# Kernel optimization log

Hardware: AMD Instinct MI355X
Metric: run time of the kernel (lower is better)

The kernel has to match this reference:

```python
import jax, jax.numpy as jnp
import numpy as np

E, N, NB = 250000, 20000, 8
D_EDGE, D_RBF, D_CBF, D_TRI = 128, 16, 16, 64
INV_SQRT_2 = 1.0 / np.sqrt(2.0).astype(np.float32)
INV_SQRT_NB = 1.0 / np.sqrt(float(NB))


def setup_inputs() -> dict:
    key = jax.random.key(0)
    ks = jax.random.split(key, 13)
    def w(k, fi, fo):
        return (jax.random.normal(k, (fi, fo), dtype=jnp.float32) / np.sqrt(fi)).astype(jnp.float32)
    return {
        "m_st": jax.random.normal(ks[0], (E, D_EDGE), dtype=jnp.float32),
        "rbf": jax.random.normal(ks[1], (E, D_RBF), dtype=jnp.float32),
        "cbf": jax.random.normal(ks[2], (E, NB, D_CBF), dtype=jnp.float32),
        "idx_s": jax.random.randint(ks[3], (E,), 0, N),
        "idx_swap": jax.random.randint(ks[4], (E,), 0, E),
        "basis_idx1": jax.random.randint(ks[5], (N, NB), 0, E),
        "W_m_rbf": w(ks[6], D_EDGE, D_EDGE),
        "W_rbf": w(ks[7], D_RBF, D_EDGE),
        "W_m_cbf": w(ks[8], D_EDGE, D_TRI),
        "W_cbf": w(ks[9], D_CBF, D_TRI),
        "W_dir": w(ks[10], D_TRI, D_EDGE),
        "W_st": w(ks[11], D_EDGE, D_EDGE),
        "W_ts": w(ks[12], D_EDGE, D_EDGE),
    }


def reference(m_st, rbf, cbf, idx_s, idx_swap, basis_idx1,
              W_m_rbf, W_rbf, W_m_cbf, W_cbf, W_dir, W_st, W_ts):
    act = jax.nn.silu
    # gather per-edge basis indices: (E, NB) -> (E*NB,)
    b1 = basis_idx1[idx_s].reshape(-1)
    # rbf branch (ScaleFactor == 1.0 at init -> identity)
    m = act(m_st @ W_m_rbf)                     # (E, D_EDGE)
    m = m * (rbf @ W_rbf)                       # (E, D_EDGE)
    # cbf branch
    e, nb, c = cbf.shape
    cbf2 = cbf.reshape(e * nb, c)               # (E*NB, D_CBF)
    m_nb = act(m @ W_m_cbf)                     # (E, D_TRI)
    m_nb = m_nb[b1]                             # gather -> (E*NB, D_TRI)
    m_nb = m_nb * (cbf2 @ W_cbf)                # (E*NB, D_TRI)
    x = m_nb.reshape(e, nb, -1).sum(1) * INV_SQRT_NB  # (E, D_TRI)
    x = act(x @ W_dir)                          # (E, D_EDGE)
    x_st = act(x @ W_st)
    x_ts = act(x @ W_ts)[idx_swap]              # swap-gather
    return (x_st + x_ts) * INV_SQRT_2
```

## Files before the change

kernel.cpp:

```cpp
#include <hip/hip_runtime.h>


#define DEV __device__ __forceinline__

typedef __attribute__((ext_vector_type(8))) short bf16x8;
typedef __attribute__((ext_vector_type(4))) float f32x4;

constexpr int E = 250000;
constexpr float INV_SQRT_2  = 0.70710678118654752f;
constexpr float INV_SQRT_NB = 0.35355339059327373f;

constexpr int PW1 = 0;
constexpr int PW2 = 16384;
constexpr int PW3 = 20480;
constexpr int PWD = 28672;
constexpr int PWS = 36864;
constexpr int PWT = 53248;
constexpr int PWC = 69632;
constexpr int PACK_TOTAL = 72192;

constexpr size_t OFF_T = 1u << 18;
constexpr size_t OFF_Z = OFF_T + (size_t)E * 64 * 2;
constexpr size_t WS_NEED_FAST = OFF_Z + (size_t)E * 128 * 4;

DEV unsigned short f2bf(float f) {
  unsigned u = __float_as_uint(f);
  return (unsigned short)((u + 0x7fffu + ((u >> 16) & 1u)) >> 16);
}
DEV float bf2f(unsigned short h) { return __uint_as_float((unsigned)h << 16); }
DEV float silu_f(float x) { return x / (1.f + __expf(-x)); }

__global__ __launch_bounds__(256) void k0_pack(
    const float* __restrict__ W1, const float* __restrict__ W2,
    const float* __restrict__ W3, const float* __restrict__ Wc,
    const float* __restrict__ Wd, const float* __restrict__ Ws,
    const float* __restrict__ Wt, unsigned short* __restrict__ pack) {
  int idx = blockIdx.x * 256 + threadIdx.x;
  if (idx >= PACK_TOTAL) return;
  float v = 0.f;
  if (idx < PW2)      { int i = idx;       int n = i >> 7, k = i & 127; v = W1[k * 128 + n]; }
  else if (idx < PW3) { int i = idx - PW2; int n = i >> 5, k = i & 31;  v = (k < 16) ? W2[k * 128 + n] : 0.f; }
  else if (idx < PWD) { int i = idx - PW3; int n = i >> 7, k = i & 127; v = W3[k * 64 + n]; }
  else if (idx < PWS) { int i = idx - PWD; int n = i >> 6, k = i & 63;  v = Wd[k * 128 + n]; }
  else if (idx < PWT) { int i = idx - PWS; int n = i >> 7, k = i & 127; v = Ws[k * 128 + n]; }
  else if (idx < PWC) { int i = idx - PWT; int n = i >> 7, k = i & 127; v = Wt[k * 128 + n]; }
  else                { int i = idx - PWC; int n = i / 40, k = i % 40;  v = (k < 16) ? Wc[k * 64 + n] : 0.f; }
  pack[idx] = f2bf(v);
}

__global__ __launch_bounds__(512) void k1_mbranch(
    const float* __restrict__ m_st, const float* __restrict__ rbf,
    const unsigned short* __restrict__ pack, unsigned short* __restrict__ tT) {
  __shared__ __align__(16) unsigned short sA[128 * 136];
  __shared__ __align__(16) unsigned short sR[128 * 40];
  const int tid = threadIdx.x;
  const int e0 = blockIdx.x * 128;

  #pragma unroll
  for (int it = 0; it < 16; ++it) {
    int i = tid + it * 512;
    int row = i >> 6, kh = i & 63;
    int er = min(e0 + row, E - 1);
    const float2 v = *(const float2*)(m_st + (size_t)er * 128 + kh * 2);
    unsigned pk = (unsigned)f2bf(v.x) | ((unsigned)f2bf(v.y) << 16);
    *(unsigned*)(sA + row * 136 + kh * 2) = pk;
  }
  #pragma unroll
  for (int it = 0; it < 4; ++it) {
    int i = tid + it * 512;
    int row = i >> 4, kh = i & 15;
    int er = min(e0 + row, E - 1);
    unsigned pk = 0;
    if (kh < 8) {
      const float2 v = *(const float2*)(rbf + (size_t)er * 16 + kh * 2);
      pk = (unsigned)f2bf(v.x) | ((unsigned)f2bf(v.y) << 16);
    }
    *(unsigned*)(sR + row * 40 + kh * 2) = pk;
  }
  __syncthreads();

  const int lane = tid & 63, wv = tid >> 6;
  const int m = lane & 15, q = lane >> 4;
  const int arow = wv * 16 + m;

  const f32x4 zero4 = {0.f, 0.f, 0.f, 0.f};
  f32x4 macc[8], racc[8];
  #pragma unroll
  for (int nt = 0; nt < 8; ++nt) { macc[nt] = zero4; racc[nt] = zero4; }

  {
    bf16x8 a = *(const bf16x8*)(sR + arow * 40 + q * 8);
    #pragma unroll
    for (int nt = 0; nt < 8; ++nt) {
      bf16x8 b = *(const bf16x8*)(pack + PW2 + (nt * 16 + m) * 32 + q * 8);
      racc[nt] = __builtin_amdgcn_mfma_f32_16x16x32_bf16(a, b, racc[nt], 0, 0, 0);
    }
  }
  #pragma unroll
  for (int kk = 0; kk < 4; ++kk) {
    bf16x8 a = *(const bf16x8*)(sA + arow * 136 + kk * 32 + q * 8);
    #pragma unroll
    for (int nt = 0; nt < 8; ++nt) {
      bf16x8 b = *(const bf16x8*)(pack + PW1 + (nt * 16 + m) * 128 + kk * 32 + q * 8);
      macc[nt] = __builtin_amdgcn_mfma_f32_16x16x32_bf16(a, b, macc[nt], 0, 0, 0);
    }
  }
  #pragma unroll
  for (int nt = 0; nt < 8; ++nt)
    #pragma unroll
    for (int r = 0; r < 4; ++r) {
      float v = silu_f(macc[nt][r]) * racc[nt][r];
      sA[(wv * 16 + q * 4 + r) * 136 + nt * 16 + m] = f2bf(v);
    }
  __syncthreads();

  f32x4 tacc[4];
  #pragma unroll
  for (int nt = 0; nt < 4; ++nt) tacc[nt] = zero4;
  #pragma unroll
  for (int kk = 0; kk < 4; ++kk) {
    bf16x8 a = *(const bf16x8*)(sA + arow * 136 + kk * 32 + q * 8);
    #pragma unroll
    for (int nt = 0; nt < 4; ++nt) {
      bf16x8 b = *(const bf16x8*)(pack + PW3 + (nt * 16 + m) * 128 + kk * 32 + q * 8);
      tacc[nt] = __builtin_amdgcn_mfma_f32_16x16x32_bf16(a, b, tacc[nt], 0, 0, 0);
    }
  }
  #pragma unroll
  for (int r = 0; r < 4; ++r) {
    int erow = e0 + wv * 16 + q * 4 + r;
    if (erow < E) {
      ushort4 o;
      o.x = f2bf(silu_f(tacc[0][r]));
      o.y = f2bf(silu_f(tacc[1][r]));
      o.z = f2bf(silu_f(tacc[2][r]));
      o.w = f2bf(silu_f(tacc[3][r]));
      *(ushort4*)(tT + (size_t)erow * 64 + m * 4) = o;
    }
  }
}

DEV void xtile_gather_reduce(
    const float* __restrict__ cbf, const int* __restrict__ sB,
    const unsigned short* __restrict__ tT, const bf16x8* bw,
    unsigned short* __restrict__ sX,
    int wv, int m, int q, long long rowA, long long rowB, int mt) {
  bf16x8 af = {0, 0, 0, 0, 0, 0, 0, 0};
  if (q < 2) {
    long long row = (m < 8) ? rowA + m : rowB + (m - 8);
    const float4 c0 = *(const float4*)(cbf + row * 16 + q * 8);
    const float4 c1 = *(const float4*)(cbf + row * 16 + q * 8 + 4);
    af[0] = (short)f2bf(c0.x); af[1] = (short)f2bf(c0.y);
    af[2] = (short)f2bf(c0.z); af[3] = (short)f2bf(c0.w);
    af[4] = (short)f2bf(c1.x); af[5] = (short)f2bf(c1.y);
    af[6] = (short)f2bf(c1.z); af[7] = (short)f2bf(c1.w);
  }
  const f32x4 zero4 = {0.f, 0.f, 0.f, 0.f};
  f32x4 p0 = zero4, p1 = zero4, p2 = zero4, p3 = zero4;
  p0 = __builtin_amdgcn_mfma_f32_16x16x32_bf16(af, bw[0], p0, 0, 0, 0);
  p1 = __builtin_amdgcn_mfma_f32_16x16x32_bf16(af, bw[1], p1, 0, 0, 0);
  p2 = __builtin_amdgcn_mfma_f32_16x16x32_bf16(af, bw[2], p2, 0, 0, 0);
  p3 = __builtin_amdgcn_mfma_f32_16x16x32_bf16(af, bw[3], p3, 0, 0, 0);

  float s0 = 0.f, s1 = 0.f, s2 = 0.f, s3 = 0.f;
  const int lrb = wv * 128 + mt * 16;
  #pragma unroll
  for (int r = 0; r < 4; ++r) {
    int brow = sB[lrb + q * 4 + r];
    ushort4 tv = *(const ushort4*)(tT + (size_t)brow * 64 + m * 4);
    s0 += bf2f(tv.x) * p0[r];
    s1 += bf2f(tv.y) * p1[r];
    s2 += bf2f(tv.z) * p2[r];
    s3 += bf2f(tv.w) * p3[r];
  }
  s0 += __shfl_xor(s0, 16);
  s1 += __shfl_xor(s1, 16);
  s2 += __shfl_xor(s2, 16);
  s3 += __shfl_xor(s3, 16);

  int lrow = wv * 16 + mt * 2 + (q >> 1);
  if (q == 0 || q == 2) {
    sX[lrow * 72 +  0 + m] = f2bf(s0 * INV_SQRT_NB);
    sX[lrow * 72 + 16 + m] = f2bf(s1 * INV_SQRT_NB);
    sX[lrow * 72 + 32 + m] = f2bf(s2 * INV_SQRT_NB);
    sX[lrow * 72 + 48 + m] = f2bf(s3 * INV_SQRT_NB);
  }
}

DEV void ytile(const unsigned short* __restrict__ pack,
               const unsigned short* __restrict__ sX,
               unsigned short* __restrict__ sY, int wv, int m, int q) {
  const int arow = wv * 16 + m;
  const f32x4 zero4 = {0.f, 0.f, 0.f, 0.f};
  f32x4 yacc[8];
  #pragma unroll
  for (int nt = 0; nt < 8; ++nt) yacc[nt] = zero4;
  #pragma unroll
  for (int kk = 0; kk < 2; ++kk) {
    bf16x8 a = *(const bf16x8*)(sX + arow * 72 + kk * 32 + q * 8);
    #pragma unroll
    for (int nt = 0; nt < 8; ++nt) {
      bf16x8 b = *(const bf16x8*)(pack + PWD + (nt * 16 + m) * 64 + kk * 32 + q * 8);
      yacc[nt] = __builtin_amdgcn_mfma_f32_16x16x32_bf16(a, b, yacc[nt], 0, 0, 0);
    }
  }
  #pragma unroll
  for (int nt = 0; nt < 8; ++nt)
    #pragma unroll
    for (int r = 0; r < 4; ++r)
      sY[(wv * 16 + q * 4 + r) * 136 + nt * 16 + m] = f2bf(silu_f(yacc[nt][r]));
}

__global__ __launch_bounds__(512) void k2_fused(
    const float* __restrict__ cbf, const int* __restrict__ idx_s,
    const int* __restrict__ basis_idx1, const unsigned short* __restrict__ pack,
    const unsigned short* __restrict__ tT, float* __restrict__ out,
    float* __restrict__ zbuf) {
  __shared__ __align__(16) unsigned short sWc[64 * 40];
  __shared__ int sB1[1024];
  __shared__ __align__(16) unsigned short sX[128 * 72];
  __shared__ __align__(16) unsigned short sY[128 * 136];
  const int tid = threadIdx.x;
  const int e0 = blockIdx.x * 128;

  ((uint2*)sWc)[tid] = ((const uint2*)(pack + PWC))[tid];
  if (tid < 128) ((uint2*)sWc)[512 + tid] = ((const uint2*)(pack + PWC))[512 + tid];
  #pragma unroll
  for (int it = 0; it < 2; ++it) {
    int i = tid + it * 512;
    int e = min(e0 + (i >> 3), E - 1);
    int b = basis_idx1[idx_s[e] * 8 + (i & 7)];
    sB1[i] = min(max(b, 0), E - 1);
  }
  __syncthreads();

  const int lane = tid & 63, wv = tid >> 6;
  const int m = lane & 15, q = lane >> 4;

  bf16x8 bw[4];
  #pragma unroll
  for (int nt = 0; nt < 4; ++nt)
    bw[nt] = *(const bf16x8*)(sWc + (nt * 16 + m) * 40 + q * 8);

  for (int mt = 0; mt < 8; ++mt) {
    int ea = min(e0 + wv * 16 + mt * 2, E - 1);
    int eb = min(ea + 1, E - 1);
    xtile_gather_reduce(cbf, sB1, tT, bw, sX, wv, m, q,
                        (long long)ea * 8, (long long)eb * 8, mt);
  }
  __syncthreads();

  ytile(pack, sX, sY, wv, m, q);
  __syncthreads();

  const int arow = wv * 16 + m;
  const f32x4 zero4 = {0.f, 0.f, 0.f, 0.f};
  f32x4 acc[8];
  #pragma unroll
  for (int nt = 0; nt < 8; ++nt) acc[nt] = zero4;
  #pragma unroll
  for (int kk = 0; kk < 4; ++kk) {
    bf16x8 a = *(const bf16x8*)(sY + arow * 136 + kk * 32 + q * 8);
    #pragma unroll
    for (int nt = 0; nt < 8; ++nt) {
      bf16x8 b = *(const bf16x8*)(pack + PWS + (nt * 16 + m) * 128 + kk * 32 + q * 8);
      acc[nt] = __builtin_amdgcn_mfma_f32_16x16x32_bf16(a, b, acc[nt], 0, 0, 0);
    }
  }
  #pragma unroll
  for (int nt = 0; nt < 8; ++nt)
    #pragma unroll
    for (int r = 0; r < 4; ++r) {
      int erow = e0 + wv * 16 + q * 4 + r;
      if (erow < E) out[(size_t)erow * 128 + nt * 16 + m] = silu_f(acc[nt][r]);
    }

  if (zbuf) {
    #pragma unroll
    for (int nt = 0; nt < 8; ++nt) acc[nt] = zero4;
    #pragma unroll
    for (int kk = 0; kk < 4; ++kk) {
      bf16x8 a = *(const bf16x8*)(sY + arow * 136 + kk * 32 + q * 8);
      #pragma unroll
      for (int nt = 0; nt < 8; ++nt) {
        bf16x8 b = *(const bf16x8*)(pack + PWT + (nt * 16 + m) * 128 + kk * 32 + q * 8);
        acc[nt] = __builtin_amdgcn_mfma_f32_16x16x32_bf16(a, b, acc[nt], 0, 0, 0);
      }
    }
    #pragma unroll
    for (int nt = 0; nt < 8; ++nt)
      #pragma unroll
      for (int r = 0; r < 4; ++r) {
        int erow = e0 + wv * 16 + q * 4 + r;
        if (erow < E) zbuf[(size_t)erow * 128 + nt * 16 + m] = silu_f(acc[nt][r]);
      }
  }
}

__global__ __launch_bounds__(256) void k3_combine(
    const int* __restrict__ idx_swap, const float* __restrict__ zbuf,
    float* __restrict__ out) {
  int t = blockIdx.x * 256 + threadIdx.x;
  int e = t >> 5, c = t & 31;
  if (e >= E) return;
  int f = idx_swap[e];
  f = min(max(f, 0), E - 1);
  float4 o = ((const float4*)out)[t];
  float4 z = ((const float4*)zbuf)[(size_t)f * 32 + c];
  o.x = (o.x + z.x) * INV_SQRT_2;
  o.y = (o.y + z.y) * INV_SQRT_2;
  o.z = (o.z + z.z) * INV_SQRT_2;
  o.w = (o.w + z.w) * INV_SQRT_2;
  ((float4*)out)[t] = o;
}

__global__ __launch_bounds__(512) void k3_swap(
    const float* __restrict__ cbf, const int* __restrict__ idx_s,
    const int* __restrict__ idx_swap, const int* __restrict__ basis_idx1,
    const unsigned short* __restrict__ pack, const unsigned short* __restrict__ tT,
    float* __restrict__ out) {
  __shared__ __align__(16) unsigned short sWc[64 * 40];
  __shared__ int sSE[128];
  __shared__ int sB3[1024];
  __shared__ __align__(16) unsigned short sX[128 * 72];
  __shared__ __align__(16) unsigned short sY[128 * 136];
  const int tid = threadIdx.x;
  const int e0 = blockIdx.x * 128;

  ((uint2*)sWc)[tid] = ((const uint2*)(pack + PWC))[tid];
  if (tid < 128) {
    ((uint2*)sWc)[512 + tid] = ((const uint2*)(pack + PWC))[512 + tid];
    int f = idx_swap[min(e0 + tid, E - 1)];
    sSE[tid] = min(max(f, 0), E - 1);
  }
  __syncthreads();
  #pragma unroll
  for (int it = 0; it < 2; ++it) {
    int i = tid + it * 512;
    int f = sSE[i >> 3];
    int b = basis_idx1[idx_s[f] * 8 + (i & 7)];
    sB3[i] = min(max(b, 0), E - 1);
  }
  __syncthreads();

  const int lane = tid & 63, wv = tid >> 6;
  const int m = lane & 15, q = lane >> 4;

  bf16x8 bw[4];
  #pragma unroll
  for (int nt = 0; nt < 4; ++nt)
    bw[nt] = *(const bf16x8*)(sWc + (nt * 16 + m) * 40 + q * 8);

  for (int mt = 0; mt < 8; ++mt) {
    int le = wv * 16 + mt * 2;
    long long fa = sSE[le], fb = sSE[le + 1];
    xtile_gather_reduce(cbf, sB3, tT, bw, sX, wv, m, q, fa * 8, fb * 8, mt);
  }
  __syncthreads();

  ytile(pack, sX, sY, wv, m, q);
  __syncthreads();

  const int arow = wv * 16 + m;
  const f32x4 zero4 = {0.f, 0.f, 0.f, 0.f};
  f32x4 acc[8];
  #pragma unroll
  for (int nt = 0; nt < 8; ++nt) acc[nt] = zero4;
  #pragma unroll
  for (int kk = 0; kk < 4; ++kk) {
    bf16x8 a = *(const bf16x8*)(sY + arow * 136 + kk * 32 + q * 8);
    #pragma unroll
    for (int nt = 0; nt < 8; ++nt) {
      bf16x8 b = *(const bf16x8*)(pack + PWT + (nt * 16 + m) * 128 + kk * 32 + q * 8);
      acc[nt] = __builtin_amdgcn_mfma_f32_16x16x32_bf16(a, b, acc[nt], 0, 0, 0);
    }
  }
  #pragma unroll
  for (int nt = 0; nt < 8; ++nt)
    #pragma unroll
    for (int r = 0; r < 4; ++r) {
      int erow = e0 + wv * 16 + q * 4 + r;
      if (erow < E) {
        size_t o = (size_t)erow * 128 + nt * 16 + m;
        out[o] = (out[o] + silu_f(acc[nt][r])) * INV_SQRT_2;
      }
    }
}

extern "C" void kernel_launch(void* const* d_in, const int* in_sizes, int n_in,
                              void* d_out, int out_size, void* d_ws, size_t ws_size,
                              hipStream_t stream) {
  const float* m_st = (const float*)d_in[0];
  const float* rbf  = (const float*)d_in[1];
  const float* cbf  = (const float*)d_in[2];
  const int* idx_s  = (const int*)d_in[3];
  const int* idx_sw = (const int*)d_in[4];
  const int* bidx   = (const int*)d_in[5];
  const float* W1 = (const float*)d_in[6];
  const float* W2 = (const float*)d_in[7];
  const float* W3 = (const float*)d_in[8];
  const float* Wc = (const float*)d_in[9];
  const float* Wd = (const float*)d_in[10];
  const float* Ws = (const float*)d_in[11];
  const float* Wt = (const float*)d_in[12];

  unsigned short* pack = (unsigned short*)d_ws;
  unsigned short* tT   = (unsigned short*)((char*)d_ws + OFF_T);
  float* zbuf = (ws_size >= WS_NEED_FAST) ? (float*)((char*)d_ws + OFF_Z) : nullptr;
  float* out = (float*)d_out;

  const int nb = (E + 127) / 128;
  k0_pack<<<(PACK_TOTAL + 255) / 256, 256, 0, stream>>>(W1, W2, W3, Wc, Wd, Ws, Wt, pack);
  k1_mbranch<<<nb, 512, 0, stream>>>(m_st, rbf, pack, tT);
  k2_fused<<<nb, 512, 0, stream>>>(cbf, idx_s, bidx, pack, tT, out, zbuf);
  if (zbuf) {
    k3_combine<<<(E * 32 + 255) / 256, 256, 0, stream>>>(idx_sw, zbuf, out);
  } else {
    k3_swap<<<nb, 512, 0, stream>>>(cbf, idx_s, idx_sw, bidx, pack, tT, out);
  }
}
```

Before: 655.1 us.

## Software-pipeline gather loads in k2 and widen k1 staging loads

The gather-reduce loop in k2 is split into an issue phase (cbf and tT gather loads) and a compute phase. Loads are double-buffered two tiles ahead so their latency overlaps the MFMA and reduction work of the current tile. k2 also gets a launch-bounds occupancy hint, and k1 stages m_st and rbf with float4 loads instead of float2. The prefetch buffers raise register pressure, and the occupancy hint may force spills.

```diff
diff --git a/kernel.cpp b/kernel.cpp
--- a/kernel.cpp
+++ b/kernel.cpp
@@ -57,25 +57,24 @@
   const int e0 = blockIdx.x * 128;
 
   #pragma unroll
-  for (int it = 0; it < 16; ++it) {
+  for (int it = 0; it < 8; ++it) {
     int i = tid + it * 512;
-    int row = i >> 6, kh = i & 63;
+    int row = i >> 5, kh = i & 31;
     int er = min(e0 + row, E - 1);
-    const float2 v = *(const float2*)(m_st + (size_t)er * 128 + kh * 2);
-    unsigned pk = (unsigned)f2bf(v.x) | ((unsigned)f2bf(v.y) << 16);
-    *(unsigned*)(sA + row * 136 + kh * 2) = pk;
-  }
-  #pragma unroll
-  for (int it = 0; it < 4; ++it) {
-    int i = tid + it * 512;
-    int row = i >> 4, kh = i & 15;
+    const float4 v = *(const float4*)(m_st + (size_t)er * 128 + kh * 4);
+    ushort4 o;
+    o.x = f2bf(v.x); o.y = f2bf(v.y); o.z = f2bf(v.z); o.w = f2bf(v.w);
+    *(ushort4*)(sA + row * 136 + kh * 4) = o;
+  }
+  {
+    int row = tid >> 2, kh = tid & 3;
     int er = min(e0 + row, E - 1);
-    unsigned pk = 0;
-    if (kh < 8) {
-      const float2 v = *(const float2*)(rbf + (size_t)er * 16 + kh * 2);
-      pk = (unsigned)f2bf(v.x) | ((unsigned)f2bf(v.y) << 16);
-    }
-    *(unsigned*)(sR + row * 40 + kh * 2) = pk;
+    const float4 v = *(const float4*)(rbf + (size_t)er * 16 + kh * 4);
+    ushort4 o;
+    o.x = f2bf(v.x); o.y = f2bf(v.y); o.z = f2bf(v.z); o.w = f2bf(v.w);
+    *(ushort4*)(sR + row * 40 + kh * 4) = o;
+    uint2 zz = {0u, 0u};
+    *(uint2*)(sR + row * 40 + 16 + kh * 4) = zz;
   }
   __syncthreads();
 
@@ -140,16 +139,30 @@
   }
 }
 
-DEV void xtile_gather_reduce(
-    const float* __restrict__ cbf, const int* __restrict__ sB,
-    const unsigned short* __restrict__ tT, const bf16x8* bw,
-    unsigned short* __restrict__ sX,
-    int wv, int m, int q, long long rowA, long long rowB, int mt) {
+DEV void x_issue(const float* __restrict__ cbf, const int* __restrict__ sB,
+                 const unsigned short* __restrict__ tT,
+                 int wv, int m, int q, int mt, long long rowA, long long rowB,
+                 float4& c0, float4& c1, ushort4* tv) {
+  if (q < 2) {
+    long long row = (m < 8) ? rowA + m : rowB + (m - 8);
+    c0 = *(const float4*)(cbf + row * 16 + q * 8);
+    c1 = *(const float4*)(cbf + row * 16 + q * 8 + 4);
+  }
+  const int lrb = wv * 128 + mt * 16 + q * 4;
+  #pragma unroll
+  for (int r = 0; r < 4; ++r) {
+    int brow = sB[lrb + r];
+    tv[r] = *(const ushort4*)(tT + (size_t)brow * 64 + m * 4);
+  }
+}
+
+DEV void x_compute(const bf16x8* bw, unsigned short* __restrict__ sX,
+                   int wv, int m, int q, int mt,
+                   const float4& c0, const float4& c1,
+                   const ushort4& tv0, const ushort4& tv1,
+                   const ushort4& tv2, const ushort4& tv3) {
   bf16x8 af = {0, 0, 0, 0, 0, 0, 0, 0};
   if (q < 2) {
-    long long row = (m < 8) ? rowA + m : rowB + (m - 8);
-    const float4 c0 = *(const float4*)(cbf + row * 16 + q * 8);
-    const float4 c1 = *(const float4*)(cbf + row * 16 + q * 8 + 4);
     af[0] = (short)f2bf(c0.x); af[1] = (short)f2bf(c0.y);
     af[2] = (short)f2bf(c0.z); af[3] = (short)f2bf(c0.w);
     af[4] = (short)f2bf(c1.x); af[5] = (short)f2bf(c1.y);
@@ -162,17 +175,11 @@
   p2 = __builtin_amdgcn_mfma_f32_16x16x32_bf16(af, bw[2], p2, 0, 0, 0);
   p3 = __builtin_amdgcn_mfma_f32_16x16x32_bf16(af, bw[3], p3, 0, 0, 0);
 
-  float s0 = 0.f, s1 = 0.f, s2 = 0.f, s3 = 0.f;
-  const int lrb = wv * 128 + mt * 16;
-  #pragma unroll
-  for (int r = 0; r < 4; ++r) {
-    int brow = sB[lrb + q * 4 + r];
-    ushort4 tv = *(const ushort4*)(tT + (size_t)brow * 64 + m * 4);
-    s0 += bf2f(tv.x) * p0[r];
-    s1 += bf2f(tv.y) * p1[r];
-    s2 += bf2f(tv.z) * p2[r];
-    s3 += bf2f(tv.w) * p3[r];
-  }
+  float s0 = bf2f(tv0.x) * p0[0] + bf2f(tv1.x) * p0[1] + bf2f(tv2.x) * p0[2] + bf2f(tv3.x) * p0[3];
+  float s1 = bf2f(tv0.y) * p1[0] + bf2f(tv1.y) * p1[1] + bf2f(tv2.y) * p1[2] + bf2f(tv3.y) * p1[3];
+  float s2 = bf2f(tv0.z) * p2[0] + bf2f(tv1.z) * p2[1] + bf2f(tv2.z) * p2[2] + bf2f(tv3.z) * p2[3];
+  float s3 = bf2f(tv0.w) * p3[0] + bf2f(tv1.w) * p3[1] + bf2f(tv2.w) * p3[2] + bf2f(tv3.w) * p3[3];
+
   s0 += __shfl_xor(s0, 16);
   s1 += __shfl_xor(s1, 16);
   s2 += __shfl_xor(s2, 16);
@@ -187,6 +194,17 @@
   }
 }
 
+DEV void xtile_gather_reduce(
+    const float* __restrict__ cbf, const int* __restrict__ sB,
+    const unsigned short* __restrict__ tT, const bf16x8* bw,
+    unsigned short* __restrict__ sX,
+    int wv, int m, int q, long long rowA, long long rowB, int mt) {
+  float4 c0, c1;
+  ushort4 tv[4];
+  x_issue(cbf, sB, tT, wv, m, q, mt, rowA, rowB, c0, c1, tv);
+  x_compute(bw, sX, wv, m, q, mt, c0, c1, tv[0], tv[1], tv[2], tv[3]);
+}
+
 DEV void ytile(const unsigned short* __restrict__ pack,
                const unsigned short* __restrict__ sX,
                unsigned short* __restrict__ sY, int wv, int m, int q) {
@@ -211,7 +229,7 @@
       sY[(wv * 16 + q * 4 + r) * 136 + nt * 16 + m] = f2bf(silu_f(yacc[nt][r]));
 }
 
-__global__ __launch_bounds__(512) void k2_fused(
+__global__ __launch_bounds__(512, 4) void k2_fused(
     const float* __restrict__ cbf, const int* __restrict__ idx_s,
     const int* __restrict__ basis_idx1, const unsigned short* __restrict__ pack,
     const unsigned short* __restrict__ tT, float* __restrict__ out,
@@ -242,11 +260,27 @@
   for (int nt = 0; nt < 4; ++nt)
     bw[nt] = *(const bf16x8*)(sWc + (nt * 16 + m) * 40 + q * 8);
 
+  float4 pc0[2], pc1[2];
+  ushort4 ptv[2][4];
+  {
+    int ea = min(e0 + wv * 16, E - 1), eb = min(ea + 1, E - 1);
+    x_issue(cbf, sB1, tT, wv, m, q, 0, (long long)ea * 8, (long long)eb * 8,
+            pc0[0], pc1[0], ptv[0]);
+    ea = min(e0 + wv * 16 + 2, E - 1); eb = min(ea + 1, E - 1);
+    x_issue(cbf, sB1, tT, wv, m, q, 1, (long long)ea * 8, (long long)eb * 8,
+            pc0[1], pc1[1], ptv[1]);
+  }
+  #pragma unroll
   for (int mt = 0; mt < 8; ++mt) {
-    int ea = min(e0 + wv * 16 + mt * 2, E - 1);
-    int eb = min(ea + 1, E - 1);
-    xtile_gather_reduce(cbf, sB1, tT, bw, sX, wv, m, q,
-                        (long long)ea * 8, (long long)eb * 8, mt);
+    const int s = mt & 1;
+    float4 c0 = pc0[s], c1 = pc1[s];
+    ushort4 tv0 = ptv[s][0], tv1 = ptv[s][1], tv2 = ptv[s][2], tv3 = ptv[s][3];
+    if (mt + 2 < 8) {
+      int ea = min(e0 + wv * 16 + (mt + 2) * 2, E - 1), eb = min(ea + 1, E - 1);
+      x_issue(cbf, sB1, tT, wv, m, q, mt + 2, (long long)ea * 8, (long long)eb * 8,
+              pc0[s], pc1[s], ptv[s]);
+    }
+    x_compute(bw, sX, wv, m, q, mt, c0, c1, tv0, tv1, tv2, tv3);
   }
   __syncthreads();
 
```

Result: faster. 634.0 us (-3.2%).
